# Kernel tuning notes

Hardware: AMD Instinct MI355X
Metric: run time of the kernel (lower is better)

## Reference

```python
import jax, jax.numpy as jnp
import numpy as np

N = 50000
IN_CH = 256
HID = 16
HEADS = 4
OUT_CH = 40
E = 800000
NEG_SLOPE = 0.2


def gat_layer(x, src, dst, W, a_src, a_dst, b, heads, out_ch, concat):
    n = x.shape[0]
    h = (x @ W).reshape(n, heads, out_ch)               # [N, H, C]
    al_src = jnp.einsum('nhc,hc->nh', h, a_src)          # [N, H]
    al_dst = jnp.einsum('nhc,hc->nh', h, a_dst)
    e = jax.nn.leaky_relu(al_src[src] + al_dst[dst], NEG_SLOPE)  # [E, H]
    m = jax.ops.segment_max(e, dst, num_segments=n)      # per-dst max for stability
    e = jnp.exp(e - m[dst])
    denom = jax.ops.segment_sum(e, dst, num_segments=n)
    alpha = e / (denom[dst] + 1e-16)                     # segment softmax [E, H]
    msg = h[src] * alpha[:, :, None]                     # [E, H, C]
    out = jax.ops.segment_sum(msg, dst, num_segments=n)  # [N, H, C]
    out = out.reshape(n, heads * out_ch) if concat else out.mean(axis=1)
    return out + b


def setup_inputs() -> dict:
    key = jax.random.key(0)
    ks = jax.random.split(key, 10)
    glorot = lambda k, shape: jax.random.normal(k, shape, jnp.float32) * np.sqrt(2.0 / (shape[0] + shape[-1]))
    return {
        'x': jax.random.normal(ks[0], (N, IN_CH), jnp.float32),
        'edge_index': jax.random.randint(ks[1], (2, E), 0, N, jnp.int64),
        'W1': glorot(ks[2], (IN_CH, HEADS * HID)),
        'a_src1': glorot(ks[3], (HEADS, HID)),
        'a_dst1': glorot(ks[4], (HEADS, HID)),
        'b1': jnp.zeros((HEADS * HID,), jnp.float32),
        'W2': glorot(ks[5], (HEADS * HID, OUT_CH)),
        'a_src2': glorot(ks[6], (1, OUT_CH)),
        'a_dst2': glorot(ks[7], (1, OUT_CH)),
        'b2': jnp.zeros((OUT_CH,), jnp.float32),
    }


def reference(x, edge_index, W1, a_src1, a_dst1, b1, W2, a_src2, a_dst2, b2):
    n = x.shape[0]
    loops = jnp.arange(n, dtype=edge_index.dtype)
    src = jnp.concatenate([edge_index[0], loops])  # PyG GATConv adds self-loops
    dst = jnp.concatenate([edge_index[1], loops])
    h = gat_layer(x, src, dst, W1, a_src1, a_dst1, b1, HEADS, HID, concat=True)
    h = jax.nn.elu(h)
    out = gat_layer(h, src, dst, W2, a_src2, a_dst2, b2, 1, OUT_CH, concat=False)
    return jax.nn.log_softmax(out, axis=-1)
```

## Files before the change

kernel.cpp:

```cpp
#include <hip/hip_runtime.h>
#include <math.h>

static constexpr int IN_CH  = 256;
static constexpr int HD1    = 64;
static constexpr int HEADS  = 4;
static constexpr int OUT_CH = 40;
static constexpr float NEG  = 0.2f;
static constexpr int BSH    = 7;
static constexpr int BRNG   = 128;

typedef __attribute__((ext_vector_type(8))) short bf16x8;
typedef __attribute__((ext_vector_type(4))) short s16x4;
typedef __attribute__((ext_vector_type(4))) float f32x4;

static __device__ __forceinline__ short f2bf(float f) {
    union { float f; unsigned u; } v; v.f = f;
    unsigned r = v.u + 0x7FFFu + ((v.u >> 16) & 1u);
    return (short)(r >> 16);
}
static __device__ __forceinline__ float bf2f(unsigned short u) {
    union { unsigned u; float f; } v; v.u = ((unsigned)u) << 16;
    return v.f;
}
static __device__ __forceinline__ unsigned f2ord(float f) {
    unsigned u = __float_as_uint(f);
    return (u & 0x80000000u) ? ~u : (u | 0x80000000u);
}
static __device__ __forceinline__ float ord2f(unsigned k) {
    unsigned u = (k & 0x80000000u) ? (k ^ 0x80000000u) : ~k;
    return __uint_as_float(u);
}

__global__ __launch_bounds__(256) void k_zero(int* __restrict__ bmeta, unsigned* __restrict__ gmax, int B) {
    int t = blockIdx.x * 256 + threadIdx.x;
    if (t < B + 2) bmeta[t] = 0;
    if (t < 8) gmax[t] = 0u;
}

__global__ __launch_bounds__(256) void k_bhist(const int* __restrict__ dst, int* __restrict__ bcnt,
                                               int E, int B, int perBlk) {
    __shared__ int lcnt[4096];
    for (int i = threadIdx.x; i < B; i += 256) lcnt[i] = 0;
    __syncthreads();
    const int s0 = blockIdx.x * perBlk;
    const int s1 = min(s0 + perBlk, E);
    for (int i = s0 + threadIdx.x; i < s1; i += 256)
        atomicAdd(&lcnt[dst[i] >> BSH], 1);
    __syncthreads();
    for (int i = threadIdx.x; i < B; i += 256)
        if (lcnt[i]) atomicAdd(&bcnt[i], lcnt[i]);
}

__global__ __launch_bounds__(256) void k_balloc(const int* __restrict__ bcnt, int* __restrict__ ebstart,
        int* __restrict__ ebcur, int* __restrict__ sstart, int* __restrict__ totals, int B, int n) {
    int t = blockIdx.x * 256 + threadIdx.x;
    if (t < B) {
        int ec = bcnt[t];
        int nodes = min(n - (t << BSH), BRNG);
        ebstart[t] = atomicAdd(&totals[0], ec);
        ebcur[t]   = ebstart[t];
        sstart[t]  = atomicAdd(&totals[1], ec + nodes);
    }
}

__global__ __launch_bounds__(256) void k_bpart(const int* __restrict__ ei, int* __restrict__ ebcur,
        uint2* __restrict__ ebuf, int E, int B, int perBlk) {
    __shared__ int lcnt[4096];
    __shared__ int lofs[4096];
    for (int i = threadIdx.x; i < B; i += 256) lcnt[i] = 0;
    __syncthreads();
    const int s0 = blockIdx.x * perBlk;
    const int s1 = min(s0 + perBlk, E);
    for (int i = s0 + threadIdx.x; i < s1; i += 256)
        atomicAdd(&lcnt[ei[E + i] >> BSH], 1);
    __syncthreads();
    for (int i = threadIdx.x; i < B; i += 256) {
        const int c = lcnt[i];
        lofs[i] = c ? atomicAdd(&ebcur[i], c) : 0;
        lcnt[i] = 0;
    }
    __syncthreads();
    for (int i = s0 + threadIdx.x; i < s1; i += 256) {
        const int d = ei[E + i], s = ei[i];
        const int b = d >> BSH;
        const int r = atomicAdd(&lcnt[b], 1);
        ebuf[lofs[b] + r] = make_uint2((unsigned)s, (unsigned)d);
    }
}

__global__ __launch_bounds__(256) void k_bcsr(const uint2* __restrict__ ebuf,
        const int* __restrict__ ebstart, const int* __restrict__ bcnt, const int* __restrict__ sstart,
        int* __restrict__ rowstart, int* __restrict__ counts, int* __restrict__ ssrc, int n) {
    __shared__ int ncnt[BRNG], rloc[BRNG], cur[BRNG];
    const int b = blockIdx.x;
    const int t = threadIdx.x;
    const int n0 = b << BSH;
    const int nodes = min(n - n0, BRNG);
    const int ec = bcnt[b];
    const int e0 = ebstart[b];
    const int s0 = sstart[b];

    if (t < BRNG) ncnt[t] = (t < nodes) ? 1 : 0;
    __syncthreads();
    for (int i = t; i < ec; i += 256)
        atomicAdd(&ncnt[ebuf[e0 + i].y & (BRNG - 1)], 1);
    __syncthreads();

    if (t < BRNG) rloc[t] = ncnt[t];
    __syncthreads();
    #pragma unroll
    for (int off = 1; off < BRNG; off <<= 1) {
        int u = 0;
        if (t < BRNG && t >= off) u = rloc[t - off];
        __syncthreads();
        if (t < BRNG) rloc[t] += u;
        __syncthreads();
    }

    if (t < nodes) {
        const int ex = rloc[t] - ncnt[t];
        rowstart[n0 + t] = s0 + ex;
        counts[n0 + t]   = ncnt[t];
        ssrc[s0 + ex]    = n0 + t;
        cur[t] = ex + 1;
    }
    __syncthreads();
    for (int i = t; i < ec; i += 256) {
        const uint2 e = ebuf[e0 + i];
        const int lo = (int)e.y & (BRNG - 1);
        const int p = atomicAdd(&cur[lo], 1);
        ssrc[s0 + p] = (int)e.x;
    }
}

__global__ __launch_bounds__(256) void k_xform1(const float* __restrict__ x,
        const float* __restrict__ W1, const float* __restrict__ a_src, const float* __restrict__ a_dst,
        unsigned short* __restrict__ h1b, float* __restrict__ alsrc, float* __restrict__ aldst,
        unsigned* __restrict__ gmax, int n)
{
    __shared__ short W1T[64][264];
    __shared__ float wmax[4][4];
    const int t = threadIdx.x;
    const int l = t & 63;
    const int w = t >> 6;

    {
        const int c = l;
        #pragma unroll
        for (int i = 0; i < 16; ++i) {
            const int kb = i * 16 + w * 4;
            s16x4 pk;
            pk[0] = f2bf(W1[(kb + 0) * 64 + c]);
            pk[1] = f2bf(W1[(kb + 1) * 64 + c]);
            pk[2] = f2bf(W1[(kb + 2) * 64 + c]);
            pk[3] = f2bf(W1[(kb + 3) * 64 + c]);
            *(s16x4*)&W1T[c][kb] = pk;
        }
    }
    __syncthreads();

    const int r0 = blockIdx.x * 64 + w * 16;
    const int lr = l & 15;
    const int lk = l >> 4;

    f32x4 acc[4];
    #pragma unroll
    for (int ct = 0; ct < 4; ++ct) acc[ct] = (f32x4){0.f, 0.f, 0.f, 0.f};

    int rowA = r0 + lr; if (rowA > n - 1) rowA = n - 1;
    const float* xrow = x + (size_t)rowA * IN_CH + lk * 8;

    float4 a0 = *(const float4*)(xrow);
    float4 a1 = *(const float4*)(xrow + 4);

    for (int ks = 0; ks < 8; ++ks) {
        bf16x8 bfrag[4];
        #pragma unroll
        for (int ct = 0; ct < 4; ++ct)
            bfrag[ct] = *(const bf16x8*)&W1T[ct * 16 + lr][ks * 32 + lk * 8];

        const float4 c0 = a0, c1 = a1;
        if (ks < 7) {
            a0 = *(const float4*)(xrow + (ks + 1) * 32);
            a1 = *(const float4*)(xrow + (ks + 1) * 32 + 4);
        }
        bf16x8 afrag;
        afrag[0] = f2bf(c0.x); afrag[1] = f2bf(c0.y);
        afrag[2] = f2bf(c0.z); afrag[3] = f2bf(c0.w);
        afrag[4] = f2bf(c1.x); afrag[5] = f2bf(c1.y);
        afrag[6] = f2bf(c1.z); afrag[7] = f2bf(c1.w);

        #pragma unroll
        for (int ct = 0; ct < 4; ++ct)
            acc[ct] = __builtin_amdgcn_mfma_f32_16x16x32_bf16(afrag, bfrag[ct], acc[ct], 0, 0, 0);
    }

    #pragma unroll
    for (int ct = 0; ct < 4; ++ct) {
        #pragma unroll
        for (int reg = 0; reg < 4; ++reg) {
            const int row = r0 + lk * 4 + reg;
            if (row < n) h1b[(size_t)row * HD1 + ct * 16 + lr] = (unsigned short)f2bf(acc[ct][reg]);
        }
    }

    float asv[4], adv[4];
    #pragma unroll
    for (int ct = 0; ct < 4; ++ct) { asv[ct] = a_src[ct * 16 + lr]; adv[ct] = a_dst[ct * 16 + lr]; }

    float mh[4] = {-1e30f, -1e30f, -1e30f, -1e30f};
    #pragma unroll
    for (int reg = 0; reg < 4; ++reg) {
        const int row = r0 + lk * 4 + reg;
        #pragma unroll
        for (int ct = 0; ct < 4; ++ct) {
            float s1 = acc[ct][reg] * asv[ct];
            float s2 = acc[ct][reg] * adv[ct];
            s1 += __shfl_xor(s1, 1); s1 += __shfl_xor(s1, 2);
            s1 += __shfl_xor(s1, 4); s1 += __shfl_xor(s1, 8);
            s2 += __shfl_xor(s2, 1); s2 += __shfl_xor(s2, 2);
            s2 += __shfl_xor(s2, 4); s2 += __shfl_xor(s2, 8);
            mh[ct] = fmaxf(mh[ct], s1);
            if (lr == 0 && row < n) {
                alsrc[row * HEADS + ct] = s1;
                aldst[row * HEADS + ct] = s2;
            }
        }
    }
    #pragma unroll
    for (int ct = 0; ct < 4; ++ct) {
        mh[ct] = fmaxf(mh[ct], __shfl_xor(mh[ct], 16));
        mh[ct] = fmaxf(mh[ct], __shfl_xor(mh[ct], 32));
    }
    if (l == 0) { wmax[w][0] = mh[0]; wmax[w][1] = mh[1]; wmax[w][2] = mh[2]; wmax[w][3] = mh[3]; }
    __syncthreads();
    if (t < 4) {
        float m = fmaxf(fmaxf(wmax[0][t], wmax[1][t]), fmaxf(wmax[2][t], wmax[3][t]));
        atomicMax(&gmax[t], f2ord(m));
    }
}

__global__ __launch_bounds__(256) void k_aggr1(const unsigned short* __restrict__ h1b,
        const float* __restrict__ alsrc, const float* __restrict__ aldst, const float* __restrict__ b1,
        const int* __restrict__ rowstart, const int* __restrict__ counts, const int* __restrict__ ssrc,
        const unsigned* __restrict__ gmax, float* __restrict__ hact, int n)
{
    const int wid  = (blockIdx.x * blockDim.x + threadIdx.x) >> 6;
    const int lane = threadIdx.x & 63;
    const int sub  = lane & 15;
    const int head = sub >> 2;

    int nid = wid * 4 + (lane >> 4);
    const bool valid = nid < n;
    if (!valid) nid = n - 1;

    const int rs  = rowstart[nid];
    const int cnt = valid ? counts[nid] : 0;

    int maxcnt = cnt;
    maxcnt = max(maxcnt, __shfl_xor(maxcnt, 16));
    maxcnt = max(maxcnt, __shfl_xor(maxcnt, 32));

    const float adB = aldst[nid * HEADS + head];
    float m = adB + ord2f(gmax[head]);
    m = m > 0.f ? m : NEG * m;

    float d = 0.f;
    float4 acc = make_float4(0.f, 0.f, 0.f, 0.f);
    for (int i0 = 0; i0 < maxcnt; i0 += 4) {
        int  sv[4]; bool on[4];
        #pragma unroll
        for (int u = 0; u < 4; ++u) {
            const int i = i0 + u;
            on[u] = i < cnt;
            sv[u] = on[u] ? ssrc[rs + i] : 0;
        }
        ushort4 hv[4]; float lv[4];
        #pragma unroll
        for (int u = 0; u < 4; ++u) {
            hv[u] = *(const ushort4*)(h1b + (size_t)sv[u] * HD1 + sub * 4);
            lv[u] = alsrc[sv[u] * HEADS + head];
        }
        #pragma unroll
        for (int u = 0; u < 4; ++u) {
            float l = lv[u] + adB;
            l = l > 0.f ? l : NEG * l;
            const float p = on[u] ? __expf(l - m) : 0.f;
            d += p;
            acc.x = fmaf(p, bf2f(hv[u].x), acc.x);
            acc.y = fmaf(p, bf2f(hv[u].y), acc.y);
            acc.z = fmaf(p, bf2f(hv[u].z), acc.z);
            acc.w = fmaf(p, bf2f(hv[u].w), acc.w);
        }
    }

    const float inv = 1.f / (d + 1e-16f);
    const float4 bv = *(const float4*)(b1 + sub * 4);
    float4 v;
    v.x = acc.x * inv + bv.x;  v.y = acc.y * inv + bv.y;
    v.z = acc.z * inv + bv.z;  v.w = acc.w * inv + bv.w;
    v.x = v.x > 0.f ? v.x : __expf(v.x) - 1.f;
    v.y = v.y > 0.f ? v.y : __expf(v.y) - 1.f;
    v.z = v.z > 0.f ? v.z : __expf(v.z) - 1.f;
    v.w = v.w > 0.f ? v.w : __expf(v.w) - 1.f;
    if (valid) *(float4*)(hact + (size_t)nid * HD1 + sub * 4) = v;
}

__global__ __launch_bounds__(64) void k_xform2(const float* __restrict__ hin,
        const float* __restrict__ W2, const float* __restrict__ a_src, const float* __restrict__ a_dst,
        unsigned short* __restrict__ h2b, float* __restrict__ alsrc, float* __restrict__ aldst,
        unsigned* __restrict__ gmax, int n)
{
    __shared__ float Ws[HD1 * OUT_CH];
    const int t = threadIdx.x;
    #pragma unroll
    for (int i = 0; i < 10; ++i) ((float4*)Ws)[i * 64 + t] = ((const float4*)W2)[i * 64 + t];
    __syncthreads();

    const int r0 = blockIdx.x * 64 + t;
    const bool valid = r0 < n;
    const int r = valid ? r0 : n - 1;

    float acc[OUT_CH];
    #pragma unroll
    for (int j = 0; j < OUT_CH; ++j) acc[j] = 0.f;

    const float4* hr = (const float4*)(hin + (size_t)r * HD1);
    for (int kq = 0; kq < 16; ++kq) {
        const float4 xv = hr[kq];
        #pragma unroll
        for (int kk = 0; kk < 4; ++kk) {
            const float xs = (kk == 0) ? xv.x : (kk == 1) ? xv.y : (kk == 2) ? xv.z : xv.w;
            const float* wrow = Ws + (kq * 4 + kk) * OUT_CH;
            #pragma unroll
            for (int jq = 0; jq < 10; ++jq) {
                const float4 w = *(const float4*)(wrow + jq * 4);
                acc[jq * 4 + 0] = fmaf(xs, w.x, acc[jq * 4 + 0]);
                acc[jq * 4 + 1] = fmaf(xs, w.y, acc[jq * 4 + 1]);
                acc[jq * 4 + 2] = fmaf(xs, w.z, acc[jq * 4 + 2]);
                acc[jq * 4 + 3] = fmaf(xs, w.w, acc[jq * 4 + 3]);
            }
        }
    }

    float s1 = 0.f, s2 = 0.f;
    #pragma unroll
    for (int jq = 0; jq < 10; ++jq) {
        const float4 av = ((const float4*)a_src)[jq];
        const float4 dv = ((const float4*)a_dst)[jq];
        s1 += acc[jq*4+0] * av.x + acc[jq*4+1] * av.y + acc[jq*4+2] * av.z + acc[jq*4+3] * av.w;
        s2 += acc[jq*4+0] * dv.x + acc[jq*4+1] * dv.y + acc[jq*4+2] * dv.z + acc[jq*4+3] * dv.w;
        if (valid) {
            ushort4 pk;
            pk.x = (unsigned short)f2bf(acc[jq*4+0]);
            pk.y = (unsigned short)f2bf(acc[jq*4+1]);
            pk.z = (unsigned short)f2bf(acc[jq*4+2]);
            pk.w = (unsigned short)f2bf(acc[jq*4+3]);
            *(ushort4*)(h2b + (size_t)r * OUT_CH + jq * 4) = pk;
        }
    }
    if (valid) { alsrc[r] = s1; aldst[r] = s2; }

    float mred = s1;
    #pragma unroll
    for (int off = 1; off < 64; off <<= 1) mred = fmaxf(mred, __shfl_xor(mred, off));
    if (t == 0) atomicMax(&gmax[4], f2ord(mred));
}

__global__ __launch_bounds__(256) void k_aggr2(const unsigned short* __restrict__ h2b,
        const float* __restrict__ alsrc, const float* __restrict__ aldst, const float* __restrict__ b2,
        const int* __restrict__ rowstart, const int* __restrict__ counts, const int* __restrict__ ssrc,
        const unsigned* __restrict__ gmax, float* __restrict__ out, int n)
{
    const int wid  = (blockIdx.x * blockDim.x + threadIdx.x) >> 6;
    const int lane = threadIdx.x & 63;
    const int sub  = lane & 15;
    const bool act = sub < 10;
    const int subc = act ? sub : 0;

    int nid = wid * 4 + (lane >> 4);
    const bool valid = nid < n;
    if (!valid) nid = n - 1;

    const int rs  = rowstart[nid];
    const int cnt = valid ? counts[nid] : 0;

    int maxcnt = cnt;
    maxcnt = max(maxcnt, __shfl_xor(maxcnt, 16));
    maxcnt = max(maxcnt, __shfl_xor(maxcnt, 32));

    const float ad = aldst[nid];
    float m = ad + ord2f(gmax[4]);
    m = m > 0.f ? m : NEG * m;

    float d = 0.f;
    float4 acc = make_float4(0.f, 0.f, 0.f, 0.f);
    for (int i0 = 0; i0 < maxcnt; i0 += 4) {
        int  sv[4]; bool on[4];
        #pragma unroll
        for (int u = 0; u < 4; ++u) {
            const int i = i0 + u;
            on[u] = i < cnt;
            sv[u] = on[u] ? ssrc[rs + i] : 0;
        }
        ushort4 hv[4]; float lv[4];
        #pragma unroll
        for (int u = 0; u < 4; ++u) {
            hv[u] = *(const ushort4*)(h2b + (size_t)sv[u] * OUT_CH + subc * 4);
            lv[u] = alsrc[sv[u]];
        }
        #pragma unroll
        for (int u = 0; u < 4; ++u) {
            float l = lv[u] + ad;
            l = l > 0.f ? l : NEG * l;
            const float p = on[u] ? __expf(l - m) : 0.f;
            d += p;
            acc.x = fmaf(p, bf2f(hv[u].x), acc.x);
            acc.y = fmaf(p, bf2f(hv[u].y), acc.y);
            acc.z = fmaf(p, bf2f(hv[u].z), acc.z);
            acc.w = fmaf(p, bf2f(hv[u].w), acc.w);
        }
    }

    const float inv = 1.f / (d + 1e-16f);
    const float4 bv = *(const float4*)(b2 + subc * 4);
    float4 v;
    v.x = acc.x * inv + bv.x;  v.y = acc.y * inv + bv.y;
    v.z = acc.z * inv + bv.z;  v.w = acc.w * inv + bv.w;

    float mv = act ? fmaxf(fmaxf(v.x, v.y), fmaxf(v.z, v.w)) : -1e30f;
    #pragma unroll
    for (int off = 1; off < 16; off <<= 1) mv = fmaxf(mv, __shfl_xor(mv, off));
    float ex = act ? (__expf(v.x - mv) + __expf(v.y - mv) + __expf(v.z - mv) + __expf(v.w - mv)) : 0.f;
    #pragma unroll
    for (int off = 1; off < 16; off <<= 1) ex += __shfl_xor(ex, off);
    const float lse = mv + __logf(ex);

    if (valid && act) {
        *(float4*)(out + (size_t)nid * OUT_CH + sub * 4) =
            make_float4(v.x - lse, v.y - lse, v.z - lse, v.w - lse);
    }
}

extern "C" void kernel_launch(void* const* d_in, const int* in_sizes, int n_in,
                              void* d_out, int out_size, void* d_ws, size_t ws_size,
                              hipStream_t stream) {
    const float* x      = (const float*)d_in[0];
    const int*   ei     = (const int*)d_in[1];
    const float* W1     = (const float*)d_in[2];
    const float* a_src1 = (const float*)d_in[3];
    const float* a_dst1 = (const float*)d_in[4];
    const float* b1     = (const float*)d_in[5];
    const float* W2     = (const float*)d_in[6];
    const float* a_src2 = (const float*)d_in[7];
    const float* a_dst2 = (const float*)d_in[8];
    const float* b2     = (const float*)d_in[9];
    float* out = (float*)d_out;

    const int N = in_sizes[0] / IN_CH;
    const int E = in_sizes[1] / 2;
    const int B = (N + BRNG - 1) >> BSH;

    char* p = (char*)d_ws;
    auto alloc = [&](size_t bytes) -> void* {
        void* r = (void*)p;
        p += (bytes + 255) & ~(size_t)255;
        return r;
    };
    int*   counts   = (int*)alloc((size_t)N * 4);
    int*   rowstart = (int*)alloc((size_t)N * 4);
    int*   ssrc     = (int*)alloc((size_t)(E + N) * 4);
    int*   bmeta    = (int*)alloc((size_t)(B + 2) * 4);
    int*   ebstart  = (int*)alloc((size_t)B * 4);
    int*   ebcur    = (int*)alloc((size_t)B * 4);
    int*   sstart   = (int*)alloc((size_t)B * 4);
    unsigned* gmax  = (unsigned*)alloc(8 * 4);
    unsigned short* h1b = (unsigned short*)alloc((size_t)N * HD1 * 2);
    unsigned short* h2b = (unsigned short*)alloc((size_t)N * OUT_CH * 2);
    float* alsrc1   = (float*)alloc((size_t)N * HEADS * 4);
    float* aldst1   = (float*)alloc((size_t)N * HEADS * 4);
    float* hact     = (float*)alloc((size_t)N * HD1 * 4);
    uint2* ebuf     = (uint2*)hact;
    int* bcnt   = bmeta;
    int* totals = bmeta + B;
    float* alsrc2 = alsrc1; float* aldst2 = aldst1;

    const int perBlk = 8192;
    const int nblkE  = (E + perBlk - 1) / perBlk;
    const int nblk64 = (N + 63) / 64;
    const int nblkAg = (N + 15) / 16;

    k_zero  <<<(B + 2 + 255) / 256, 256, 0, stream>>>(bmeta, gmax, B);
    k_bhist <<<nblkE, 256, 0, stream>>>(ei + E, bcnt, E, B, perBlk);
    k_balloc<<<(B + 255) / 256, 256, 0, stream>>>(bcnt, ebstart, ebcur, sstart, totals, B, N);
    k_bpart <<<nblkE, 256, 0, stream>>>(ei, ebcur, ebuf, E, B, perBlk);
    k_bcsr  <<<B, 256, 0, stream>>>(ebuf, ebstart, bcnt, sstart, rowstart, counts, ssrc, N);

    k_xform1 <<<nblk64, 256, 0, stream>>>(x, W1, a_src1, a_dst1, h1b, alsrc1, aldst1, gmax, N);
    k_aggr1  <<<nblkAg, 256, 0, stream>>>(h1b, alsrc1, aldst1, b1, rowstart, counts, ssrc, gmax, hact, N);
    k_xform2 <<<nblk64, 64, 0, stream>>>(hact, W2, a_src2, a_dst2, h2b, alsrc2, aldst2, gmax, N);
    k_aggr2  <<<nblkAg, 256, 0, stream>>>(h2b, alsrc2, aldst2, b2, rowstart, counts, ssrc, gmax, out, N);
}
```

Baseline: 160.7 us.

## Fuse layer-2 linear transform into layer-1 aggregation kernel

The layer-1 aggregation kernel now stages each node's ELU output row in shared memory and immediately multiplies it by W2 (kept in LDS), writing bf16 h2 plus the layer-2 attention logits and the global max. This removes the k_xform2 launch and the round trip of the fp32 hidden activation through global memory. The cost is extra LDS use and block-wide syncs in the aggregation kernel, which may reduce occupancy. alsrc2/aldst2 and ebuf now get their own buffers instead of aliasing.

```diff
diff --git a/kernel.cpp b/kernel.cpp
--- a/kernel.cpp
+++ b/kernel.cpp
@@ -243,10 +243,19 @@
 __global__ __launch_bounds__(256) void k_aggr1(const unsigned short* __restrict__ h1b,
         const float* __restrict__ alsrc, const float* __restrict__ aldst, const float* __restrict__ b1,
         const int* __restrict__ rowstart, const int* __restrict__ counts, const int* __restrict__ ssrc,
-        const unsigned* __restrict__ gmax, float* __restrict__ hact, int n)
+        const float* __restrict__ W2, const float* __restrict__ a_src2, const float* __restrict__ a_dst2,
+        unsigned* __restrict__ gmax,
+        unsigned short* __restrict__ h2b, float* __restrict__ alsrc2, float* __restrict__ aldst2, int n)
 {
-    const int wid  = (blockIdx.x * blockDim.x + threadIdx.x) >> 6;
-    const int lane = threadIdx.x & 63;
+    __shared__ float W2s[HD1 * OUT_CH];
+    __shared__ float hrow[16][68];
+    __shared__ float wred[4];
+
+    const int t = threadIdx.x;
+    for (int i = t; i < 640; i += 256) ((float4*)W2s)[i] = ((const float4*)W2)[i];
+
+    const int wid  = (blockIdx.x * blockDim.x + t) >> 6;
+    const int lane = t & 63;
     const int sub  = lane & 15;
     const int head = sub >> 2;
 
@@ -303,68 +312,51 @@
     v.y = v.y > 0.f ? v.y : __expf(v.y) - 1.f;
     v.z = v.z > 0.f ? v.z : __expf(v.z) - 1.f;
     v.w = v.w > 0.f ? v.w : __expf(v.w) - 1.f;
-    if (valid) *(float4*)(hact + (size_t)nid * HD1 + sub * 4) = v;
-}
-
-__global__ __launch_bounds__(64) void k_xform2(const float* __restrict__ hin,
-        const float* __restrict__ W2, const float* __restrict__ a_src, const float* __restrict__ a_dst,
-        unsigned short* __restrict__ h2b, float* __restrict__ alsrc, float* __restrict__ aldst,
-        unsigned* __restrict__ gmax, int n)
-{
-    __shared__ float Ws[HD1 * OUT_CH];
-    const int t = threadIdx.x;
-    #pragma unroll
-    for (int i = 0; i < 10; ++i) ((float4*)Ws)[i * 64 + t] = ((const float4*)W2)[i * 64 + t];
-    __syncthreads();
-
-    const int r0 = blockIdx.x * 64 + t;
-    const bool valid = r0 < n;
-    const int r = valid ? r0 : n - 1;
-
-    float acc[OUT_CH];
-    #pragma unroll
-    for (int j = 0; j < OUT_CH; ++j) acc[j] = 0.f;
-
-    const float4* hr = (const float4*)(hin + (size_t)r * HD1);
-    for (int kq = 0; kq < 16; ++kq) {
-        const float4 xv = hr[kq];
-        #pragma unroll
-        for (int kk = 0; kk < 4; ++kk) {
-            const float xs = (kk == 0) ? xv.x : (kk == 1) ? xv.y : (kk == 2) ? xv.z : xv.w;
-            const float* wrow = Ws + (kq * 4 + kk) * OUT_CH;
-            #pragma unroll
-            for (int jq = 0; jq < 10; ++jq) {
-                const float4 w = *(const float4*)(wrow + jq * 4);
-                acc[jq * 4 + 0] = fmaf(xs, w.x, acc[jq * 4 + 0]);
-                acc[jq * 4 + 1] = fmaf(xs, w.y, acc[jq * 4 + 1]);
-                acc[jq * 4 + 2] = fmaf(xs, w.z, acc[jq * 4 + 2]);
-                acc[jq * 4 + 3] = fmaf(xs, w.w, acc[jq * 4 + 3]);
-            }
-        }
+
+    *(float4*)&hrow[t >> 4][sub * 4] = v;
+    __syncthreads();
+
+    const bool act = sub < 10;
+    const int jc = act ? sub * 4 : 0;
+    float4 h2v = make_float4(0.f, 0.f, 0.f, 0.f);
+    const float* hr = hrow[t >> 4];
+    #pragma unroll 8
+    for (int k = 0; k < 64; ++k) {
+        const float xs = hr[k];
+        const float4 wv = *(const float4*)&W2s[k * OUT_CH + jc];
+        h2v.x = fmaf(xs, wv.x, h2v.x);
+        h2v.y = fmaf(xs, wv.y, h2v.y);
+        h2v.z = fmaf(xs, wv.z, h2v.z);
+        h2v.w = fmaf(xs, wv.w, h2v.w);
     }
 
     float s1 = 0.f, s2 = 0.f;
-    #pragma unroll
-    for (int jq = 0; jq < 10; ++jq) {
-        const float4 av = ((const float4*)a_src)[jq];
-        const float4 dv = ((const float4*)a_dst)[jq];
-        s1 += acc[jq*4+0] * av.x + acc[jq*4+1] * av.y + acc[jq*4+2] * av.z + acc[jq*4+3] * av.w;
-        s2 += acc[jq*4+0] * dv.x + acc[jq*4+1] * dv.y + acc[jq*4+2] * dv.z + acc[jq*4+3] * dv.w;
+    if (act) {
+        const float4 av = *(const float4*)(a_src2 + jc);
+        const float4 dv = *(const float4*)(a_dst2 + jc);
+        s1 = h2v.x * av.x + h2v.y * av.y + h2v.z * av.z + h2v.w * av.w;
+        s2 = h2v.x * dv.x + h2v.y * dv.y + h2v.z * dv.z + h2v.w * dv.w;
         if (valid) {
             ushort4 pk;
-            pk.x = (unsigned short)f2bf(acc[jq*4+0]);
-            pk.y = (unsigned short)f2bf(acc[jq*4+1]);
-            pk.z = (unsigned short)f2bf(acc[jq*4+2]);
-            pk.w = (unsigned short)f2bf(acc[jq*4+3]);
-            *(ushort4*)(h2b + (size_t)r * OUT_CH + jq * 4) = pk;
-        }
-    }
-    if (valid) { alsrc[r] = s1; aldst[r] = s2; }
-
-    float mred = s1;
-    #pragma unroll
-    for (int off = 1; off < 64; off <<= 1) mred = fmaxf(mred, __shfl_xor(mred, off));
-    if (t == 0) atomicMax(&gmax[4], f2ord(mred));
+            pk.x = (unsigned short)f2bf(h2v.x);
+            pk.y = (unsigned short)f2bf(h2v.y);
+            pk.z = (unsigned short)f2bf(h2v.z);
+            pk.w = (unsigned short)f2bf(h2v.w);
+            *(ushort4*)(h2b + (size_t)nid * OUT_CH + jc) = pk;
+        }
+    }
+    s1 += __shfl_xor(s1, 1); s1 += __shfl_xor(s1, 2);
+    s1 += __shfl_xor(s1, 4); s1 += __shfl_xor(s1, 8);
+    s2 += __shfl_xor(s2, 1); s2 += __shfl_xor(s2, 2);
+    s2 += __shfl_xor(s2, 4); s2 += __shfl_xor(s2, 8);
+    if (valid && sub == 0) { alsrc2[nid] = s1; aldst2[nid] = s2; }
+
+    float m1 = s1;
+    m1 = fmaxf(m1, __shfl_xor(m1, 16));
+    m1 = fmaxf(m1, __shfl_xor(m1, 32));
+    if (lane == 0) wred[t >> 6] = m1;
+    __syncthreads();
+    if (t == 0) atomicMax(&gmax[4], f2ord(fmaxf(fmaxf(wred[0], wred[1]), fmaxf(wred[2], wred[3]))));
 }
 
 __global__ __launch_bounds__(256) void k_aggr2(const unsigned short* __restrict__ h2b,
@@ -479,11 +471,11 @@
     unsigned short* h2b = (unsigned short*)alloc((size_t)N * OUT_CH * 2);
     float* alsrc1   = (float*)alloc((size_t)N * HEADS * 4);
     float* aldst1   = (float*)alloc((size_t)N * HEADS * 4);
-    float* hact     = (float*)alloc((size_t)N * HD1 * 4);
-    uint2* ebuf     = (uint2*)hact;
+    float* alsrc2   = (float*)alloc((size_t)N * 4);
+    float* aldst2   = (float*)alloc((size_t)N * 4);
+    uint2* ebuf     = (uint2*)alloc((size_t)E * 8);
     int* bcnt   = bmeta;
     int* totals = bmeta + B;
-    float* alsrc2 = alsrc1; float* aldst2 = aldst1;
 
     const int perBlk = 8192;
     const int nblkE  = (E + perBlk - 1) / perBlk;
@@ -497,7 +489,7 @@
     k_bcsr  <<<B, 256, 0, stream>>>(ebuf, ebstart, bcnt, sstart, rowstart, counts, ssrc, N);
 
     k_xform1 <<<nblk64, 256, 0, stream>>>(x, W1, a_src1, a_dst1, h1b, alsrc1, aldst1, gmax, N);
-    k_aggr1  <<<nblkAg, 256, 0, stream>>>(h1b, alsrc1, aldst1, b1, rowstart, counts, ssrc, gmax, hact, N);
-    k_xform2 <<<nblk64, 64, 0, stream>>>(hact, W2, a_src2, a_dst2, h2b, alsrc2, aldst2, gmax, N);
+    k_aggr1  <<<nblkAg, 256, 0, stream>>>(h1b, alsrc1, aldst1, b1, rowstart, counts, ssrc,
+                                          W2, a_src2, a_dst2, gmax, h2b, alsrc2, aldst2, N);
     k_aggr2  <<<nblkAg, 256, 0, stream>>>(h2b, alsrc2, aldst2, b2, rowstart, counts, ssrc, gmax, out, N);
 }
```

After: 190.9 us. 18.8% more time.
